# Performance work log

Measured on AMD Instinct MI355X. Metric: run time of the kernel, lower is better.

Reference implementation:

```python
import math
import jax, jax.numpy as jnp
import numpy as np

N, L, D = 64, 128, 768          # batch, n_in capsules, feature dim
IN_DIM, OUT_DIM, N_OUT = 64, 64, 32
EPS = 1e-8

def _xavier(k, shape):
    # torch xavier_uniform: fan_in = shape[1]*prod(shape[2:]), fan_out = shape[0]*prod(shape[2:])
    rec = int(np.prod(shape[2:])) if len(shape) > 2 else 1
    fan_in, fan_out = shape[-2] * rec, shape[-1] * rec
    a = math.sqrt(6.0 / (fan_in + fan_out))
    return jax.random.uniform(k, shape, jnp.float32, -a, a)

def setup_inputs() -> dict:
    key = jax.random.key(0)
    ks = jax.random.split(key, 4)
    return {
        "x": jax.random.normal(ks[0], (N, L, D), jnp.float32),
        "Wscore": _xavier(ks[1], (L, D, 1)),
        "Bscore": jnp.zeros((L, 1, 1), jnp.float32),
        "Wcap": _xavier(ks[2], (L, D, IN_DIM)),
        "Bcap": jnp.zeros((L, 1, IN_DIM), jnp.float32),
        "Wvote": _xavier(ks[3], (L, N_OUT, IN_DIM, OUT_DIM)),
        "Bvote": jnp.zeros((L, N_OUT, 1, OUT_DIM), jnp.float32),
        "beta_use": jnp.zeros((L, 1, 1, 1), jnp.float32),
        "beta_ign": jnp.zeros((1, N_OUT, 1, 1), jnp.float32),
        "iters": 3,
    }

def reference(x, Wscore, Bscore, Wcap, Bcap, Wvote, Bvote, beta_use, beta_ign, iters):
    n_out = Wvote.shape[1]
    pi = jnp.asarray(math.pi, x.dtype)
    x_t = jnp.transpose(x, (1, 0, 2))                     # (L, N, D)
    a_in = jnp.matmul(x_t, Wscore) + Bscore               # (L, N, 1)
    mu_in = jax.nn.gelu(jnp.matmul(x_t, Wcap) + Bcap, approximate=False)  # (L, N, in_dim)
    f_a_in = jax.nn.sigmoid(a_in)[:, None, :, :]          # (L, 1, N, 1)
    # votes: (L, n_out, N, out_dim)
    V = jnp.einsum('lni,loij->lonj', mu_in, Wvote) + Bvote

    def em_step(R):
        D_use = f_a_in * R                                # (L, n_out, N, 1)
        D_ign = f_a_in - D_use
        a_out = jnp.sum(beta_use * D_use, axis=0) - jnp.sum(beta_ign * D_ign, axis=0)  # (n_out, N, 1)
        denom = jnp.sum(D_use, axis=0) + EPS              # (n_out, N, 1)
        mu_out = jnp.sum(D_use * V, axis=0) / denom       # (n_out, N, out_dim)
        var_out = jnp.sum(D_use * (V - mu_out[None]) ** 2, axis=0) / denom
        return a_out, mu_out, var_out

    R = jnp.full((1, n_out, 1, 1), 1.0 / n_out, dtype=x.dtype)
    a_out, mu_out, var_out = em_step(R)
    for _ in range(int(iters) - 1):
        # Gaussian log-likelihood of each vote under each output capsule
        log_p = (-jnp.sum((V - mu_out[None]) ** 2 / (2.0 * var_out[None] + EPS), axis=-1)
                 - 1.0 - 0.5 * pi
                 - 0.5 * jnp.sum(jnp.log(var_out[None] + EPS), axis=-1))   # (L, n_out, N)
        R = jax.nn.softmax(jax.nn.log_sigmoid(a_out)[None] + log_p[..., None], axis=1)
        a_out, mu_out, var_out = em_step(R)

    a_out = jnp.transpose(a_out[..., 0], (1, 0))          # (N, n_out)
    mu_out = jnp.transpose(mu_out, (1, 0, 2))             # (N, n_out, out_dim)
    return a_out, mu_out
```

## Files before the change

### kernel.cpp

```cpp
#include <hip/hip_runtime.h>
#include <math.h>

#define NB 64
#define LL 128
#define DD 768
#define ID 64
#define OD 64
#define NO 32
#define EPSF 1e-8f

typedef unsigned short ushort_t;
typedef __attribute__((ext_vector_type(8))) short bf16x8;
typedef __attribute__((ext_vector_type(4))) float f32x4;


__device__ __forceinline__ float gelu_exact(float v) {
  return 0.5f * v * (1.0f + erff(v * 0.70710678118654752440f));
}
__device__ __forceinline__ float sigmoidf_(float z) {
  return 1.0f / (1.0f + __expf(-z));
}
__device__ __forceinline__ unsigned short f2bf(float f) {
  unsigned u = __float_as_uint(f);
  unsigned r = (u + 0x7FFFu + ((u >> 16) & 1u)) >> 16;
  return (unsigned short)r;
}
__device__ __forceinline__ float bf2f(unsigned short s) {
  return __uint_as_float(((unsigned)s) << 16);
}

__global__ __launch_bounds__(256) void k0a_proj(
    const float* __restrict__ x, const float* __restrict__ Wscore,
    const float* __restrict__ Wcap,
    float* __restrict__ Cpart, float* __restrict__ apart)
{
  const int l  = blockIdx.x & 127;
  const int kc = blockIdx.x >> 7;
  const int t = threadIdx.x;
  const int tn = t >> 4;
  const int ti = t & 15;
  __shared__ float Xs[64][68];
  __shared__ float Ws[64][68];
  __shared__ float Ss[64];
  float C[4][4] = {{0.f}};
  float asum[4] = {0.f, 0.f, 0.f, 0.f};

  for (int kt = 0; kt < 2; ++kt) {
    const int kbase = kc * 128 + kt * 64;
#pragma unroll
    for (int r = 0; r < 4; ++r) {
      const int flat = r * 1024 + t * 4;
      const int p = flat >> 6, qq = flat & 63;
      *(float4*)&Xs[p][qq] = *(const float4*)&x[(p * LL + l) * DD + kbase + qq];
      *(float4*)&Ws[p][qq] = *(const float4*)&Wcap[(l * DD + kbase + p) * ID + qq];
    }
    if (t < 16)
      *(float4*)&Ss[4 * t] = *(const float4*)&Wscore[l * DD + kbase + 4 * t];
    __syncthreads();
#pragma unroll 8
    for (int k = 0; k < 64; ++k) {
      float av[4];
      av[0] = Xs[4 * tn + 0][k];
      av[1] = Xs[4 * tn + 1][k];
      av[2] = Xs[4 * tn + 2][k];
      av[3] = Xs[4 * tn + 3][k];
      const float4 b = *(const float4*)&Ws[k][4 * ti];
      const float sk = Ss[k];
#pragma unroll
      for (int a = 0; a < 4; ++a) {
        C[a][0] = fmaf(av[a], b.x, C[a][0]);
        C[a][1] = fmaf(av[a], b.y, C[a][1]);
        C[a][2] = fmaf(av[a], b.z, C[a][2]);
        C[a][3] = fmaf(av[a], b.w, C[a][3]);
        asum[a] = fmaf(av[a], sk, asum[a]);
      }
    }
    __syncthreads();
  }
#pragma unroll
  for (int a = 0; a < 4; ++a)
    *(float4*)&Cpart[kc * 524288 + (l * 64 + 4 * tn + a) * 64 + 4 * ti] =
        make_float4(C[a][0], C[a][1], C[a][2], C[a][3]);
  if (ti == 0) {
#pragma unroll
    for (int a = 0; a < 4; ++a)
      apart[kc * 8192 + l * 64 + 4 * tn + a] = asum[a];
  }
}

__global__ __launch_bounds__(256) void k0b_reduce(
    const float* __restrict__ Cpart, const float* __restrict__ Bcap,
    ushort_t* __restrict__ Ah, ushort_t* __restrict__ Al)
{
  const int e = (blockIdx.x * 256 + threadIdx.x) * 4;
  float4 s = *(const float4*)&Cpart[e];
#pragma unroll
  for (int kc = 1; kc < 6; ++kc) {
    const float4 p = *(const float4*)&Cpart[kc * 524288 + e];
    s.x += p.x; s.y += p.y; s.z += p.z; s.w += p.w;
  }
  const int l = e >> 12;
  const int col = e & 63;
  const float4 bc = *(const float4*)&Bcap[l * 64 + col];
  float m[4] = {gelu_exact(s.x + bc.x), gelu_exact(s.y + bc.y),
                gelu_exact(s.z + bc.z), gelu_exact(s.w + bc.w)};
  ushort4 h, lo;
  h.x = f2bf(m[0]); lo.x = f2bf(m[0] - bf2f(h.x));
  h.y = f2bf(m[1]); lo.y = f2bf(m[1] - bf2f(h.y));
  h.z = f2bf(m[2]); lo.z = f2bf(m[2] - bf2f(h.z));
  h.w = f2bf(m[3]); lo.w = f2bf(m[3] - bf2f(h.w));
  *(ushort4*)&Ah[e] = h;
  *(ushort4*)&Al[e] = lo;
}

__global__ __launch_bounds__(256) void k0c_fa(
    const float* __restrict__ apart, const float* __restrict__ Bscore,
    float* __restrict__ f_a)
{
  const int e = blockIdx.x * 256 + threadIdx.x;
  float s = 0.f;
#pragma unroll
  for (int kc = 0; kc < 6; ++kc) s += apart[kc * 8192 + e];
  const int l = e >> 6;
  f_a[e] = sigmoidf_(s + Bscore[l]);
}

__global__ __launch_bounds__(256) void k1_votes(
    const ushort_t* __restrict__ Ah, const ushort_t* __restrict__ Al,
    const float* __restrict__ Wvote, const float* __restrict__ Bvote,
    float* __restrict__ V)
{
  const int t = threadIdx.x;
  const int w = t >> 6;
  const int lane = t & 63;
  const int pair = blockIdx.x * 4 + w;
  const int l = pair >> 5;
  const int mr = lane & 15, q = lane >> 4;

  __shared__ unsigned HL_all[4][4096];
  unsigned* HL = HL_all[w];

  bf16x8 afh[2][4], afl[2][4];
#pragma unroll
  for (int ks = 0; ks < 2; ++ks)
#pragma unroll
    for (int mt = 0; mt < 4; ++mt) {
      const int off = l * 4096 + (16 * mt + mr) * 64 + ks * 32 + q * 8;
      afh[ks][mt] = *(const bf16x8*)&Ah[off];
      afl[ks][mt] = *(const bf16x8*)&Al[off];
    }

  const float* Wt = Wvote + (size_t)pair * 4096;
#pragma unroll
  for (int f = 0; f < 16; ++f) {
    const float4 v4 = *(const float4*)&Wt[f * 256 + lane * 4];
    const int i = f * 4 + q;
    const int j0 = mr * 4;
    const float e4[4] = {v4.x, v4.y, v4.z, v4.w};
    unsigned pk[4];
#pragma unroll
    for (int d = 0; d < 4; ++d) {
      const unsigned short hi = f2bf(e4[d]);
      const unsigned short lo = f2bf(e4[d] - bf2f(hi));
      pk[d] = (unsigned)hi | ((unsigned)lo << 16);
    }
    *(uint4*)&HL[i * 64 + j0] = make_uint4(pk[0], pk[1], pk[2], pk[3]);
  }

  f32x4 acc[4][4];
#pragma unroll
  for (int mt = 0; mt < 4; ++mt)
#pragma unroll
    for (int nt = 0; nt < 4; ++nt) {
      f32x4 z = {0.f, 0.f, 0.f, 0.f};
      acc[mt][nt] = z;
    }

#pragma unroll
  for (int ks = 0; ks < 2; ++ks)
#pragma unroll
    for (int nt = 0; nt < 4; ++nt) {
      const int j = 16 * nt + mr;
      const int i0 = ks * 32 + q * 8;
      unsigned wv[8];
#pragma unroll
      for (int d = 0; d < 8; ++d) wv[d] = HL[(i0 + d) * 64 + j];
      union { ushort_t u[8]; bf16x8 v; } bh, bl;
#pragma unroll
      for (int d = 0; d < 8; ++d) {
        bh.u[d] = (ushort_t)(wv[d] & 0xffffu);
        bl.u[d] = (ushort_t)(wv[d] >> 16);
      }
#pragma unroll
      for (int mt = 0; mt < 4; ++mt) {
        acc[mt][nt] = __builtin_amdgcn_mfma_f32_16x16x32_bf16(
            afh[ks][mt], bh.v, acc[mt][nt], 0, 0, 0);
        acc[mt][nt] = __builtin_amdgcn_mfma_f32_16x16x32_bf16(
            afh[ks][mt], bl.v, acc[mt][nt], 0, 0, 0);
        acc[mt][nt] = __builtin_amdgcn_mfma_f32_16x16x32_bf16(
            afl[ks][mt], bh.v, acc[mt][nt], 0, 0, 0);
      }
    }

  float bv[4];
#pragma unroll
  for (int nt = 0; nt < 4; ++nt) bv[nt] = Bvote[pair * 64 + 16 * nt + mr];

#pragma unroll
  for (int mt = 0; mt < 4; ++mt)
#pragma unroll
    for (int r = 0; r < 4; ++r) {
      const int n = 16 * mt + 4 * q + r;
      const size_t base = (size_t)n * (LL * NO * OD) + (size_t)pair * 64;
#pragma unroll
      for (int nt = 0; nt < 4; ++nt)
        V[base + 16 * nt + mr] = acc[mt][nt][r] + bv[nt];
    }
}

__global__ __launch_bounds__(256) void k3_em(
    const float* __restrict__ V, const float* __restrict__ f_a,
    const float* __restrict__ beta_use, const float* __restrict__ mu_s,
    const float* __restrict__ i2v_s, const float* __restrict__ cterm,
    float* __restrict__ S1p, float* __restrict__ S2p,
    float* __restrict__ dnp, float* __restrict__ aUp, const int mode)
{
  const int n = blockIdx.x >> 3;
  const int c = blockIdx.x & 7;
  const int t = threadIdx.x;
  const int o = t >> 3, q = t & 7;
  __shared__ float ttl[8][32];

  float mu8[8], iv8[8];
  float ct = 0.f;
  if (mode) {
    const float4 a0 = *(const float4*)&mu_s[n * 2048 + t * 8];
    const float4 a1 = *(const float4*)&mu_s[n * 2048 + t * 8 + 4];
    mu8[0] = a0.x; mu8[1] = a0.y; mu8[2] = a0.z; mu8[3] = a0.w;
    mu8[4] = a1.x; mu8[5] = a1.y; mu8[6] = a1.z; mu8[7] = a1.w;
    const float4 b0 = *(const float4*)&i2v_s[n * 2048 + t * 8];
    const float4 b1 = *(const float4*)&i2v_s[n * 2048 + t * 8 + 4];
    iv8[0] = b0.x; iv8[1] = b0.y; iv8[2] = b0.z; iv8[3] = b0.w;
    iv8[4] = b1.x; iv8[5] = b1.y; iv8[6] = b1.z; iv8[7] = b1.w;
    ct = cterm[n * NO + o];
  }
  float aS1[8] = {0.f, 0.f, 0.f, 0.f, 0.f, 0.f, 0.f, 0.f};
  float aS2[8] = {0.f, 0.f, 0.f, 0.f, 0.f, 0.f, 0.f, 0.f};
  float dn = 0.f, aU = 0.f;

  for (int g = 0; g < 4; ++g) {
    const int lb = c * 16 + g * 4;
    float Vv[4][8], fa4[4], bu4[4], tt4[4];
#pragma unroll
    for (int u = 0; u < 4; ++u) {
      const int l = lb + u;
      const float4 v0 = *(const float4*)&V[((size_t)n * LL + l) * 2048 + t * 8];
      const float4 v1 = *(const float4*)&V[((size_t)n * LL + l) * 2048 + t * 8 + 4];
      Vv[u][0] = v0.x; Vv[u][1] = v0.y; Vv[u][2] = v0.z; Vv[u][3] = v0.w;
      Vv[u][4] = v1.x; Vv[u][5] = v1.y; Vv[u][6] = v1.z; Vv[u][7] = v1.w;
      fa4[u] = f_a[l * NB + n];
      bu4[u] = beta_use[l];
    }
    if (mode) {
#pragma unroll
      for (int u = 0; u < 4; ++u) {
        float s2 = 0.f;
#pragma unroll
        for (int k = 0; k < 8; ++k) {
          const float d = Vv[u][k] - mu8[k];
          s2 = fmaf(d * d, iv8[k], s2);
        }
        s2 += __shfl_xor(s2, 1);
        s2 += __shfl_xor(s2, 2);
        s2 += __shfl_xor(s2, 4);
        tt4[u] = ct - s2;
      }
      const int sb = (g & 1) * 4;
      if (q == 0) {
#pragma unroll
        for (int u = 0; u < 4; ++u) ttl[sb + u][o] = tt4[u];
      }
      __syncthreads();
#pragma unroll
      for (int u = 0; u < 4; ++u) {
        const float vv = ttl[sb + u][t & 31];
        float m = vv;
#pragma unroll
        for (int msk = 1; msk <= 16; msk <<= 1) m = fmaxf(m, __shfl_xor(m, msk));
        float z = __expf(vv - m);
#pragma unroll
        for (int msk = 1; msk <= 16; msk <<= 1) z += __shfl_xor(z, msk);
        const float wgt = fa4[u] * __expf(tt4[u] - m) / z;
        dn += wgt;
        aU = fmaf(bu4[u], wgt, aU);
#pragma unroll
        for (int k = 0; k < 8; ++k) {
          const float d = Vv[u][k] - mu8[k];
          aS1[k] = fmaf(wgt, Vv[u][k], aS1[k]);
          aS2[k] = fmaf(wgt, d * d, aS2[k]);
        }
      }
    } else {
#pragma unroll
      for (int u = 0; u < 4; ++u) {
        const float wgt = fa4[u] * (1.0f / NO);
        dn += wgt;
        aU = fmaf(bu4[u], wgt, aU);
#pragma unroll
        for (int k = 0; k < 8; ++k) {
          aS1[k] = fmaf(wgt, Vv[u][k], aS1[k]);
          aS2[k] = fmaf(wgt * Vv[u][k], Vv[u][k], aS2[k]);
        }
      }
    }
  }
  const int base = ((c * NB + n) * NO + o) * OD + q * 8;
  *(float4*)&S1p[base]     = make_float4(aS1[0], aS1[1], aS1[2], aS1[3]);
  *(float4*)&S1p[base + 4] = make_float4(aS1[4], aS1[5], aS1[6], aS1[7]);
  *(float4*)&S2p[base]     = make_float4(aS2[0], aS2[1], aS2[2], aS2[3]);
  *(float4*)&S2p[base + 4] = make_float4(aS2[4], aS2[5], aS2[6], aS2[7]);
  if (q == 0) {
    dnp[(c * NB + n) * NO + o] = dn;
    aUp[(c * NB + n) * NO + o] = aU;
  }
}

__global__ __launch_bounds__(256) void k4_fin23(
    const float* __restrict__ S1p, const float* __restrict__ S2p,
    const float* __restrict__ dnp, const float* __restrict__ aUp,
    const float* __restrict__ f_a, const float* __restrict__ beta_ign,
    float* __restrict__ mu_s, float* __restrict__ i2v_s, float* __restrict__ cterm,
    float* __restrict__ out, const int final_iter, const int first)
{
  const int n = blockIdx.x;
  const int t = threadIdx.x;
  const int o = t >> 3, q = t & 7;
  const int j0 = q * 8;
  __shared__ float rA[128];
  if (t < 128) rA[t] = f_a[t * NB + n];
  __syncthreads();
  for (int s = 64; s >= 1; s >>= 1) {
    if (t < s) rA[t] += rA[t + s];
    __syncthreads();
  }
  const float Fsum = rA[0];

  float dn = 0.f, aU = 0.f;
#pragma unroll
  for (int cc = 0; cc < 8; ++cc) {
    dn += dnp[(cc * NB + n) * NO + o];
    aU += aUp[(cc * NB + n) * NO + o];
  }
  const float S0 = dn;
  const float denom = dn + EPSF;
  const float inv_den = 1.0f / denom;

  float S1[8], S2[8];
#pragma unroll
  for (int k = 0; k < 8; ++k) { S1[k] = 0.f; S2[k] = 0.f; }
  for (int cc = 0; cc < 8; ++cc) {
    const int base = ((cc * NB + n) * NO + o) * OD + j0;
    const float4 u0 = *(const float4*)&S1p[base];
    const float4 u1 = *(const float4*)&S1p[base + 4];
    const float4 w0 = *(const float4*)&S2p[base];
    const float4 w1 = *(const float4*)&S2p[base + 4];
    S1[0] += u0.x; S1[1] += u0.y; S1[2] += u0.z; S1[3] += u0.w;
    S1[4] += u1.x; S1[5] += u1.y; S1[6] += u1.z; S1[7] += u1.w;
    S2[0] += w0.x; S2[1] += w0.y; S2[2] += w0.z; S2[3] += w0.w;
    S2[4] += w1.x; S2[5] += w1.y; S2[6] += w1.z; S2[7] += w1.w;
  }
  float mup[8];
  if (first) {
#pragma unroll
    for (int k = 0; k < 8; ++k) mup[k] = 0.f;
  } else {
    const float4 a0 = *(const float4*)&mu_s[n * 2048 + t * 8];
    const float4 a1 = *(const float4*)&mu_s[n * 2048 + t * 8 + 4];
    mup[0] = a0.x; mup[1] = a0.y; mup[2] = a0.z; mup[3] = a0.w;
    mup[4] = a1.x; mup[5] = a1.y; mup[6] = a1.z; mup[7] = a1.w;
  }
  const float aout = aU - beta_ign[o] * (Fsum - dn);

  float mu[8], i2v[8];
  float lacc = 0.f;
#pragma unroll
  for (int k = 0; k < 8; ++k) {
    mu[k] = S1[k] * inv_den;
    const float dd = mu[k] - mup[k];
    float varn = S2[k] - 2.0f * dd * (S1[k] - mup[k] * S0) + dd * dd * S0;
    float var = fmaxf(varn * inv_den, 0.0f);
    i2v[k] = 1.0f / (2.0f * var + EPSF);
    lacc += logf(var + EPSF);
  }
  if (final_iter) {
    if (q == 0) out[n * NO + o] = aout;
    *(float4*)&out[2048 + n * 2048 + t * 8]     = make_float4(mu[0], mu[1], mu[2], mu[3]);
    *(float4*)&out[2048 + n * 2048 + t * 8 + 4] = make_float4(mu[4], mu[5], mu[6], mu[7]);
  } else {
    *(float4*)&mu_s[n * 2048 + t * 8]      = make_float4(mu[0], mu[1], mu[2], mu[3]);
    *(float4*)&mu_s[n * 2048 + t * 8 + 4]  = make_float4(mu[4], mu[5], mu[6], mu[7]);
    *(float4*)&i2v_s[n * 2048 + t * 8]     = make_float4(i2v[0], i2v[1], i2v[2], i2v[3]);
    *(float4*)&i2v_s[n * 2048 + t * 8 + 4] = make_float4(i2v[4], i2v[5], i2v[6], i2v[7]);
    lacc += __shfl_xor(lacc, 1);
    lacc += __shfl_xor(lacc, 2);
    lacc += __shfl_xor(lacc, 4);
    const float lsg = fminf(aout, 0.0f) - log1pf(__expf(-fabsf(aout)));
    if (q == 0) cterm[n * NO + o] = lsg - 0.5f * lacc;
  }
}

extern "C" void kernel_launch(void* const* d_in, const int* in_sizes, int n_in,
                              void* d_out, int out_size, void* d_ws, size_t ws_size,
                              hipStream_t stream) {
  const float* x        = (const float*)d_in[0];
  const float* Wscore   = (const float*)d_in[1];
  const float* Bscore   = (const float*)d_in[2];
  const float* Wcap     = (const float*)d_in[3];
  const float* Bcap     = (const float*)d_in[4];
  const float* Wvote    = (const float*)d_in[5];
  const float* Bvote    = (const float*)d_in[6];
  const float* beta_use = (const float*)d_in[7];
  const float* beta_ign = (const float*)d_in[8];
  float* out = (float*)d_out;

  float* ws     = (float*)d_ws;
  float* V      = ws;
  float* Cpart  = ws;
  float* apart  = ws + 3145728;
  ushort_t* Ah  = (ushort_t*)(ws + 16777216);
  ushort_t* Al  = Ah + 524288;
  float* f_a    = ws + 16777216 + 524288;
  float* S1p    = f_a + 8192;
  float* S2p    = S1p + 1048576;
  float* dnp    = S2p + 1048576;
  float* aUp    = dnp + 16384;
  float* mu_s   = aUp + 16384;
  float* i2v_s  = mu_s + 131072;
  float* ct     = i2v_s + 131072;
  const size_t need = (size_t)(16777216 + 524288 + 8192 + 2 * 1048576 +
                               2 * 16384 + 2 * 131072 + 2048) * sizeof(float);
  if (ws_size < need) return;

  k0a_proj<<<768, 256, 0, stream>>>(x, Wscore, Wcap, Cpart, apart);
  k0b_reduce<<<512, 256, 0, stream>>>(Cpart, Bcap, Ah, Al);
  k0c_fa<<<32, 256, 0, stream>>>(apart, Bscore, f_a);
  k1_votes<<<1024, 256, 0, stream>>>(Ah, Al, Wvote, Bvote, V);
  k3_em<<<512, 256, 0, stream>>>(V, f_a, beta_use, mu_s, i2v_s, ct, S1p, S2p, dnp, aUp, 0);
  k4_fin23<<<64, 256, 0, stream>>>(S1p, S2p, dnp, aUp, f_a, beta_ign, mu_s, i2v_s, ct, out, 0, 1);
  k3_em<<<512, 256, 0, stream>>>(V, f_a, beta_use, mu_s, i2v_s, ct, S1p, S2p, dnp, aUp, 1);
  k4_fin23<<<64, 256, 0, stream>>>(S1p, S2p, dnp, aUp, f_a, beta_ign, mu_s, i2v_s, ct, out, 0, 0);
  k3_em<<<512, 256, 0, stream>>>(V, f_a, beta_use, mu_s, i2v_s, ct, S1p, S2p, dnp, aUp, 1);
  k4_fin23<<<64, 256, 0, stream>>>(S1p, S2p, dnp, aUp, f_a, beta_ign, mu_s, i2v_s, ct, out, 1, 0);
}
```

Baseline: 247.3 us.

## Load vote weights directly into registers and split EM reduction into more chunks

```diff
diff --git a/kernel.cpp b/kernel.cpp
--- a/kernel.cpp
+++ b/kernel.cpp
@@ -125,7 +125,7 @@
   f_a[e] = sigmoidf_(s + Bscore[l]);
 }
 
-__global__ __launch_bounds__(256) void k1_votes(
+__global__ __launch_bounds__(256, 2) void k1_votes(
     const ushort_t* __restrict__ Ah, const ushort_t* __restrict__ Al,
     const float* __restrict__ Wvote, const float* __restrict__ Bvote,
     float* __restrict__ V)
@@ -137,9 +137,6 @@
   const int l = pair >> 5;
   const int mr = lane & 15, q = lane >> 4;
 
-  __shared__ unsigned HL_all[4][4096];
-  unsigned* HL = HL_all[w];
-
   bf16x8 afh[2][4], afl[2][4];
 #pragma unroll
   for (int ks = 0; ks < 2; ++ks)
@@ -151,21 +148,14 @@
     }
 
   const float* Wt = Wvote + (size_t)pair * 4096;
-#pragma unroll
-  for (int f = 0; f < 16; ++f) {
-    const float4 v4 = *(const float4*)&Wt[f * 256 + lane * 4];
-    const int i = f * 4 + q;
-    const int j0 = mr * 4;
-    const float e4[4] = {v4.x, v4.y, v4.z, v4.w};
-    unsigned pk[4];
-#pragma unroll
-    for (int d = 0; d < 4; ++d) {
-      const unsigned short hi = f2bf(e4[d]);
-      const unsigned short lo = f2bf(e4[d] - bf2f(hi));
-      pk[d] = (unsigned)hi | ((unsigned)lo << 16);
-    }
-    *(uint4*)&HL[i * 64 + j0] = make_uint4(pk[0], pk[1], pk[2], pk[3]);
-  }
+  float braw[2][4][8];
+#pragma unroll
+  for (int ks = 0; ks < 2; ++ks)
+#pragma unroll
+    for (int nt = 0; nt < 4; ++nt)
+#pragma unroll
+      for (int d = 0; d < 8; ++d)
+        braw[ks][nt][d] = Wt[(ks * 32 + q * 8 + d) * 64 + 16 * nt + mr];
 
   f32x4 acc[4][4];
 #pragma unroll
@@ -180,16 +170,13 @@
   for (int ks = 0; ks < 2; ++ks)
 #pragma unroll
     for (int nt = 0; nt < 4; ++nt) {
-      const int j = 16 * nt + mr;
-      const int i0 = ks * 32 + q * 8;
-      unsigned wv[8];
-#pragma unroll
-      for (int d = 0; d < 8; ++d) wv[d] = HL[(i0 + d) * 64 + j];
       union { ushort_t u[8]; bf16x8 v; } bh, bl;
 #pragma unroll
       for (int d = 0; d < 8; ++d) {
-        bh.u[d] = (ushort_t)(wv[d] & 0xffffu);
-        bl.u[d] = (ushort_t)(wv[d] >> 16);
+        const float x = braw[ks][nt][d];
+        const unsigned short hi = f2bf(x);
+        bh.u[d] = hi;
+        bl.u[d] = f2bf(x - bf2f(hi));
       }
 #pragma unroll
       for (int mt = 0; mt < 4; ++mt) {
@@ -225,8 +212,8 @@
     float* __restrict__ S1p, float* __restrict__ S2p,
     float* __restrict__ dnp, float* __restrict__ aUp, const int mode)
 {
-  const int n = blockIdx.x >> 3;
-  const int c = blockIdx.x & 7;
+  const int n = blockIdx.x >> 4;
+  const int c = blockIdx.x & 15;
   const int t = threadIdx.x;
   const int o = t >> 3, q = t & 7;
   __shared__ float ttl[8][32];
@@ -248,8 +235,8 @@
   float aS2[8] = {0.f, 0.f, 0.f, 0.f, 0.f, 0.f, 0.f, 0.f};
   float dn = 0.f, aU = 0.f;
 
-  for (int g = 0; g < 4; ++g) {
-    const int lb = c * 16 + g * 4;
+  for (int g = 0; g < 2; ++g) {
+    const int lb = c * 8 + g * 4;
     float Vv[4][8], fa4[4], bu4[4], tt4[4];
 #pragma unroll
     for (int u = 0; u < 4; ++u) {
@@ -347,7 +334,7 @@
 
   float dn = 0.f, aU = 0.f;
 #pragma unroll
-  for (int cc = 0; cc < 8; ++cc) {
+  for (int cc = 0; cc < 16; ++cc) {
     dn += dnp[(cc * NB + n) * NO + o];
     aU += aUp[(cc * NB + n) * NO + o];
   }
@@ -358,7 +345,7 @@
   float S1[8], S2[8];
 #pragma unroll
   for (int k = 0; k < 8; ++k) { S1[k] = 0.f; S2[k] = 0.f; }
-  for (int cc = 0; cc < 8; ++cc) {
+  for (int cc = 0; cc < 16; ++cc) {
     const int base = ((cc * NB + n) * NO + o) * OD + j0;
     const float4 u0 = *(const float4*)&S1p[base];
     const float4 u1 = *(const float4*)&S1p[base + 4];
@@ -431,24 +418,24 @@
   ushort_t* Al  = Ah + 524288;
   float* f_a    = ws + 16777216 + 524288;
   float* S1p    = f_a + 8192;
-  float* S2p    = S1p + 1048576;
-  float* dnp    = S2p + 1048576;
-  float* aUp    = dnp + 16384;
-  float* mu_s   = aUp + 16384;
+  float* S2p    = S1p + 2097152;
+  float* dnp    = S2p + 2097152;
+  float* aUp    = dnp + 32768;
+  float* mu_s   = aUp + 32768;
   float* i2v_s  = mu_s + 131072;
   float* ct     = i2v_s + 131072;
-  const size_t need = (size_t)(16777216 + 524288 + 8192 + 2 * 1048576 +
-                               2 * 16384 + 2 * 131072 + 2048) * sizeof(float);
+  const size_t need = (size_t)(16777216 + 524288 + 8192 + 2 * 2097152 +
+                               2 * 32768 + 2 * 131072 + 2048) * sizeof(float);
   if (ws_size < need) return;
 
   k0a_proj<<<768, 256, 0, stream>>>(x, Wscore, Wcap, Cpart, apart);
   k0b_reduce<<<512, 256, 0, stream>>>(Cpart, Bcap, Ah, Al);
   k0c_fa<<<32, 256, 0, stream>>>(apart, Bscore, f_a);
   k1_votes<<<1024, 256, 0, stream>>>(Ah, Al, Wvote, Bvote, V);
-  k3_em<<<512, 256, 0, stream>>>(V, f_a, beta_use, mu_s, i2v_s, ct, S1p, S2p, dnp, aUp, 0);
+  k3_em<<<1024, 256, 0, stream>>>(V, f_a, beta_use, mu_s, i2v_s, ct, S1p, S2p, dnp, aUp, 0);
   k4_fin23<<<64, 256, 0, stream>>>(S1p, S2p, dnp, aUp, f_a, beta_ign, mu_s, i2v_s, ct, out, 0, 1);
-  k3_em<<<512, 256, 0, stream>>>(V, f_a, beta_use, mu_s, i2v_s, ct, S1p, S2p, dnp, aUp, 1);
+  k3_em<<<1024, 256, 0, stream>>>(V, f_a, beta_use, mu_s, i2v_s, ct, S1p, S2p, dnp, aUp, 1);
   k4_fin23<<<64, 256, 0, stream>>>(S1p, S2p, dnp, aUp, f_a, beta_ign, mu_s, i2v_s, ct, out, 0, 0);
-  k3_em<<<512, 256, 0, stream>>>(V, f_a, beta_use, mu_s, i2v_s, ct, S1p, S2p, dnp, aUp, 1);
+  k3_em<<<1024, 256, 0, stream>>>(V, f_a, beta_use, mu_s, i2v_s, ct, S1p, S2p, dnp, aUp, 1);
   k4_fin23<<<64, 256, 0, stream>>>(S1p, S2p, dnp, aUp, f_a, beta_ign, mu_s, i2v_s, ct, out, 1, 0);
 }
```

After: 275.3 us. 11.3% more time.
